# Performance work log

Measured on AMD Instinct MI355X. Metric: run time of the kernel, lower is better.

Reference implementation:

```python
import jax, jax.numpy as jnp
import numpy as np

R_MAX = 6.0
N_RADIAL = 5
N_BASIS = 7
N_SPECIES = 119
N_ATOMS = 25000
N_EDGES = 1000000


def _tril_2d(n):
    return np.array([(i, j) for i in range(n) for j in range(i + 1)], dtype=np.int32)


def _tril_3d(n):
    return np.array([(i, j, k) for i in range(n) for j in range(i + 1) for k in range(j + 1)], dtype=np.int32)


TRIL2 = jnp.asarray(_tril_2d(N_RADIAL))  # [15, 2]
TRIL3 = jnp.asarray(_tril_3d(N_RADIAL))  # [35, 3]


def setup_inputs() -> dict:
    key = jax.random.key(0)
    k1, k2, k3, k4 = jax.random.split(key, 4)
    dr_vec = jax.random.normal(k1, (N_EDGES, 3), jnp.float32) * 2.0
    Z = jax.random.randint(k2, (N_ATOMS,), 0, N_SPECIES, jnp.int32)
    neighbor_idxs = jax.random.randint(k3, (2, N_EDGES), 0, N_ATOMS, jnp.int32)
    coeffs = jax.random.normal(k4, (N_SPECIES, N_SPECIES, N_RADIAL, N_BASIS), jnp.float32) * 0.1
    return {"dr_vec": dr_vec, "Z": Z, "neighbor_idxs": neighbor_idxs, "coeffs": coeffs}


def _radial(dr, Z_i, Z_j, coeffs):
    # Gaussian basis (apax-style) with species-pair linear coefficients + cosine cutoff
    betta = N_BASIS ** 2 / R_MAX ** 2
    rad_norm = (2.0 * betta / np.pi) ** 0.75
    shifts = jnp.linspace(0.0, R_MAX, N_BASIS, dtype=dr.dtype)
    basis = rad_norm * jnp.exp(-betta * (dr[:, None] - shifts[None, :]) ** 2)  # [E, B]
    cutoff = 0.5 * (jnp.cos(np.pi * dr / R_MAX) + 1.0) * (dr < R_MAX)  # [E]
    c = coeffs[Z_i, Z_j]  # [E, R, B]
    rad = jnp.einsum("eb,erb->er", basis, c) * cutoff[:, None] / np.sqrt(N_BASIS)
    return rad  # [E, R]


def _forward(dr_vec, Z, neighbor_idxs, coeffs):
    idx_i, idx_j = neighbor_idxs[0], neighbor_idxs[1]
    Z_i, Z_j = Z[idx_i], Z[idx_j]
    dr = jnp.linalg.norm(dr_vec, axis=-1)  # [E]
    dn = dr_vec / (dr + 1e-5)[:, None]  # [E, 3]
    rad = _radial(dr, Z_i, Z_j, coeffs)  # [E, R]

    # per-edge outer-product moments
    m1e = rad[..., None] * dn[:, None, :]                      # [E,R,3]
    m2e = m1e[..., None] * dn[:, None, None, :]                # [E,R,3,3]
    m3e = m2e[..., None] * dn[:, None, None, None, :]          # [E,R,3,3,3]

    seg = lambda x: jax.ops.segment_sum(x, idx_j, num_segments=N_ATOMS)
    m0 = seg(rad)   # [A,R]
    m1 = seg(m1e)   # [A,R,3]
    m2 = seg(m2e)   # [A,R,3,3]
    m3 = seg(m3e)   # [A,R,3,3,3]

    contr_0 = m0
    contr_1 = jnp.einsum("ari,asi->rsa", m1, m1)
    contr_2 = jnp.einsum("arij,asij->rsa", m2, m2)
    contr_3 = jnp.einsum("arijk,asijk->rsa", m3, m3)
    contr_4 = jnp.einsum("arij,asik,atjk->rsta", m2, m2, m2)
    contr_5 = jnp.einsum("ari,asj,atij->rsta", m1, m1, m2)
    contr_6 = jnp.einsum("arijk,asijl,atkl->rsta", m3, m3, m2)
    contr_7 = jnp.einsum("arijk,asij,atk->rsta", m3, m2, m1)

    t2i, t2j = TRIL2[:, 0], TRIL2[:, 1]
    t3i, t3j, t3k = TRIL3[:, 0], TRIL3[:, 1], TRIL3[:, 2]

    n_atoms = contr_0.shape[0]
    contr_1 = contr_1[t2i, t2j].reshape(n_atoms, -1)
    contr_2 = contr_2[t2i, t2j].reshape(n_atoms, -1)
    contr_3 = contr_3[t2i, t2j].reshape(n_atoms, -1)
    contr_4 = contr_4[t3i, t3j, t3k].reshape(n_atoms, -1)
    contr_5 = contr_5[t2i, t2j].reshape(n_atoms, -1)
    contr_6 = contr_6[t2i, t2j].reshape(n_atoms, -1)
    contr_7 = contr_7.reshape(n_atoms, -1)

    return jnp.concatenate([contr_0, contr_1, contr_2, contr_3, contr_4, contr_5, contr_6, contr_7], axis=-1)


def reference(dr_vec, Z, neighbor_idxs, coeffs):
    return _forward(dr_vec, Z, neighbor_idxs, coeffs)
```

## Files before the change

### kernel.cpp

```cpp
#include <hip/hip_runtime.h>
#include <math.h>

#define NR 5
#define NB 7
#define NS 119
#define NA 25000
#define NE 1000000
#define OC 360
#define MUS 100
#define CAPR 96
#define CAPI 112
#define CHUNK 64
#define MPAD 101
#define CROW 36

static constexpr int T2I[15] = {0,1,1,2,2,2,3,3,3,3,4,4,4,4,4};
static constexpr int T2J[15] = {0,0,1,0,1,2,0,1,2,3,0,1,2,3,4};
static constexpr int T3I[35] = {0,1,1,1,2,2,2,2,2,2,3,3,3,3,3,3,3,3,3,3,4,4,4,4,4,4,4,4,4,4,4,4,4,4,4};
static constexpr int T3J[35] = {0,0,1,1,0,1,1,2,2,2,0,1,1,2,2,2,3,3,3,3,0,1,1,2,2,2,3,3,3,3,4,4,4,4,4};
static constexpr int T3K[35] = {0,0,0,1,0,0,1,0,1,2,0,0,1,0,1,2,0,1,2,3,0,0,1,0,1,2,0,1,2,3,0,1,2,3,4};

static constexpr int P2[9]  = {0,1,2, 1,3,4, 2,4,5};
static constexpr int P3[27] = {0,1,4, 1,2,5, 4,5,7,
                               1,2,5, 2,3,6, 5,6,8,
                               4,5,7, 5,6,8, 7,8,9};
static constexpr float W2[6]  = {1.f,2.f,2.f,1.f,2.f,1.f};
static constexpr float W3[10] = {1.f,3.f,3.f,1.f,3.f,6.f,3.f,3.f,3.f,1.f};

__global__ __launch_bounds__(256) void transpose_coeffs_kernel(
    const float* __restrict__ src, float* __restrict__ dst)
{
    int t = blockIdx.x * 256 + threadIdx.x;
    const int TOT = NS * NS * (NR * NB);
    if (t >= TOT) return;
    int pair = t / 35, rem = t - pair * 35;
    dst[pair * CROW + rem] = src[t];
}

__global__ __launch_bounds__(256) void edge_record_kernel(
    const float* __restrict__ dr_vec, const int* __restrict__ Z,
    const int* __restrict__ nbr, const float* __restrict__ coeffsT,
    int* __restrict__ cursor, float* __restrict__ binrec)
{
    int e = blockIdx.x * 256 + threadIdx.x;
    if (e >= NE) return;

    int aj = nbr[NE + e];
    int pos = __hip_atomic_fetch_add(&cursor[aj], 1,
                                     __ATOMIC_RELAXED, __HIP_MEMORY_SCOPE_AGENT);

    int ai = nbr[e];
    float x = dr_vec[3*e+0], y = dr_vec[3*e+1], z = dr_vec[3*e+2];
    int Zi = Z[ai], Zj = Z[aj];

    const float4* c4 = (const float4*)(coeffsT + (size_t)(Zi*NS + Zj) * CROW);
    float4 cw[9];
#pragma unroll
    for (int k = 0; k < 9; k++) cw[k] = c4[k];
    const float* cf = (const float*)&cw[0];

    float dr  = sqrtf(x*x + y*y + z*z);
    float inv = 1.0f / (dr + 1e-5f);
    float d0 = x*inv, d1 = y*inv, d2 = z*inv;

    const float PI_F = 3.14159265358979323846f;
    const float betta = 49.0f / 36.0f;
    float rad_norm = powf(2.0f * betta / PI_F, 0.75f);
    float cut = (dr < 6.0f) ? 0.5f*(cosf(PI_F * dr * (1.0f/6.0f)) + 1.0f) : 0.0f;
    float scale = cut * 0.3779644730092272272f;

    float basis[NB];
#pragma unroll
    for (int b = 0; b < NB; b++) {
        float t = dr - (float)b;
        basis[b] = rad_norm * expf(-betta * t * t);
    }

    float rad[NR];
#pragma unroll
    for (int r = 0; r < NR; r++) {
        float s = 0.f;
#pragma unroll
        for (int b = 0; b < NB; b++) s += basis[b] * cf[r*NB + b];
        rad[r] = s * scale;
    }

    if (pos < CAPR) {
        float4* rp = (float4*)(binrec + ((size_t)aj * CAPR + pos) * 8);
        rp[0] = make_float4(rad[0], rad[1], rad[2], rad[3]);
        rp[1] = make_float4(rad[4], d0, d1, d2);
    }
}

__global__ __launch_bounds__(256) void accum_contract_kernel(
    const int* __restrict__ cursor, const float* __restrict__ binrec,
    float* __restrict__ out)
{
    __shared__ float lds[CHUNK * MPAD];
    int base = blockIdx.x * CHUNK;
    int nat  = min(CHUNK, NA - base);

    int al  = threadIdx.x >> 2;
    int sub = threadIdx.x & 3;
    int a   = base + al;
    int n   = (a < NA) ? min(cursor[a], CAPR) : 0;

    float acc[MUS];
#pragma unroll
    for (int i = 0; i < MUS; i++) acc[i] = 0.f;

    const float* mybin = binrec + (size_t)a * CAPR * 8;
    for (int p = sub; p < n; p += 4) {
        const float4* rp = (const float4*)(mybin + (size_t)p * 8);
        float4 r0 = rp[0], r1 = rp[1];
        float rad[NR] = {r0.x, r0.y, r0.z, r0.w, r1.x};
        float d0 = r1.y, d1 = r1.z, d2 = r1.w;

        float q2[6] = {d0*d0, d1*d0, d2*d0, d1*d1, d2*d1, d2*d2};
        float q3[10] = {d0*q2[0], d1*q2[0], d0*q2[3], d1*q2[3], d2*q2[0],
                        d2*q2[1], d2*q2[3], d0*q2[5], d1*q2[5], d2*q2[5]};

#pragma unroll
        for (int r = 0; r < NR; r++) {
            float rv = rad[r];
            acc[r] += rv;
            acc[5 + r*3 + 0] += rv*d0;
            acc[5 + r*3 + 1] += rv*d1;
            acc[5 + r*3 + 2] += rv*d2;
#pragma unroll
            for (int q = 0; q < 6; q++)  acc[20 + r*6  + q] += rv*q2[q];
#pragma unroll
            for (int q = 0; q < 10; q++) acc[50 + r*10 + q] += rv*q3[q];
        }
    }

#pragma unroll
    for (int i = 0; i < MUS; i++) {
        float v = acc[i];
        v += __shfl_xor(v, 1, 64);
        v += __shfl_xor(v, 2, 64);
        if (sub == 0) lds[al * MPAD + i] = v;
    }
    __syncthreads();

    int wave = threadIdx.x >> 6, lane = threadIdx.x & 63;
    int a2 = base + lane;
    bool valid = (lane < nat);
    int mb = lane * MPAD;

#define ML(o) lds[mb + (o)]

    for (int cc = wave; cc < 360; cc += 4) {
        if (!valid) continue;
        float v; int dest;

        if (cc < 5) {
            v = ML(cc);
            dest = a2 * OC + cc;
        } else if (cc < 20) {
            int l = cc - 5;
            int r = T2I[l], s = T2J[l];
            float acc2 = 0.f;
#pragma unroll
            for (int i = 0; i < 3; i++) acc2 += ML(5 + r*3 + i) * ML(5 + s*3 + i);
            v = acc2;
            int f = l * NA + a2; int aa = f / 15; dest = aa * OC + 5 + (f - aa*15);
        } else if (cc < 35) {
            int l = cc - 20;
            int r = T2I[l], s = T2J[l];
            float acc2 = 0.f;
#pragma unroll
            for (int p = 0; p < 6; p++) acc2 += W2[p] * ML(20 + r*6 + p) * ML(20 + s*6 + p);
            v = acc2;
            int f = l * NA + a2; int aa = f / 15; dest = aa * OC + 20 + (f - aa*15);
        } else if (cc < 50) {
            int l = cc - 35;
            int r = T2I[l], s = T2J[l];
            float acc2 = 0.f;
#pragma unroll
            for (int p = 0; p < 10; p++) acc2 += W3[p] * ML(50 + r*10 + p) * ML(50 + s*10 + p);
            v = acc2;
            int f = l * NA + a2; int aa = f / 15; dest = aa * OC + 35 + (f - aa*15);
        } else if (cc < 85) {
            int l = cc - 50;
            int r = T3I[l], s = T3J[l], t = T3K[l];
            float R[6], S[6], T[6];
#pragma unroll
            for (int p = 0; p < 6; p++) { R[p]=ML(20+r*6+p); S[p]=ML(20+s*6+p); T[p]=ML(20+t*6+p); }
            float acc2 = 0.f;
#pragma unroll
            for (int i = 0; i < 3; i++)
#pragma unroll
            for (int j = 0; j < 3; j++)
#pragma unroll
            for (int k = 0; k < 3; k++)
                acc2 += R[P2[i*3+j]] * S[P2[i*3+k]] * T[P2[j*3+k]];
            v = acc2;
            int f = l * NA + a2; int aa = f / 35; dest = aa * OC + 50 + (f - aa*35);
        } else if (cc < 160) {
            int l = cc - 85;
            int p = l / 5, t = l - p*5;
            int r = T2I[p], s = T2J[p];
            float T[6];
#pragma unroll
            for (int q = 0; q < 6; q++) T[q] = ML(20 + t*6 + q);
            float acc2 = 0.f;
#pragma unroll
            for (int i = 0; i < 3; i++)
#pragma unroll
            for (int j = 0; j < 3; j++)
                acc2 += ML(5 + r*3 + i) * ML(5 + s*3 + j) * T[P2[i*3+j]];
            v = acc2;
            int f = l * NA + a2; int aa = f / 75; dest = aa * OC + 85 + (f - aa*75);
        } else if (cc < 235) {
            int l = cc - 160;
            int p = l / 5, t = l - p*5;
            int r = T2I[p], s = T2J[p];
            float R[10], S[10], T[6];
#pragma unroll
            for (int q = 0; q < 10; q++) { R[q]=ML(50+r*10+q); S[q]=ML(50+s*10+q); }
#pragma unroll
            for (int q = 0; q < 6;  q++) T[q] = ML(20 + t*6 + q);
            float acc2 = 0.f;
#pragma unroll
            for (int k = 0; k < 3; k++)
#pragma unroll
            for (int l2 = 0; l2 < 3; l2++) {
                float inner = 0.f;
#pragma unroll
                for (int i = 0; i < 3; i++)
#pragma unroll
                for (int j = 0; j < 3; j++)
                    inner += R[P3[(i*3+j)*3+k]] * S[P3[(i*3+j)*3+l2]];
                acc2 += inner * T[P2[k*3+l2]];
            }
            v = acc2;
            int f = l * NA + a2; int aa = f / 75; dest = aa * OC + 160 + (f - aa*75);
        } else {
            int l = cc - 235;
            int r = l / 25; int rem = l - r*25; int s = rem / 5; int t = rem - s*5;
            float R[10], S[6], T1[3];
#pragma unroll
            for (int q = 0; q < 10; q++) R[q] = ML(50 + r*10 + q);
#pragma unroll
            for (int q = 0; q < 6;  q++) S[q] = ML(20 + s*6 + q);
#pragma unroll
            for (int q = 0; q < 3;  q++) T1[q] = ML(5 + t*3 + q);
            float acc2 = 0.f;
#pragma unroll
            for (int i = 0; i < 3; i++)
#pragma unroll
            for (int j = 0; j < 3; j++)
#pragma unroll
            for (int k = 0; k < 3; k++)
                acc2 += R[P3[(i*3+j)*3+k]] * S[P2[i*3+j]] * T1[k];
            v = acc2;
            int f = l * NA + a2; int aa = f / 125; dest = aa * OC + 235 + (f - aa*125);
        }
        out[dest] = v;
    }
#undef ML
}

__global__ __launch_bounds__(256) void scatter_kernel(
    const int* __restrict__ nbr, int* __restrict__ cursor, int* __restrict__ bins)
{
    int e = blockIdx.x * 256 + threadIdx.x;
    if (e >= NE) return;
    int aj = nbr[NE + e];
    int pos = __hip_atomic_fetch_add(&cursor[aj], 1, __ATOMIC_RELAXED, __HIP_MEMORY_SCOPE_AGENT);
    if (pos < CAPI) bins[(size_t)aj * CAPI + pos] = e;
}

__global__ __launch_bounds__(256) void accum_kernel(
    const float* __restrict__ dr_vec, const int* __restrict__ Z,
    const int* __restrict__ nbr, const float* __restrict__ coeffs,
    const int* __restrict__ cursor, const int* __restrict__ bins,
    float* __restrict__ Mu)
{
    __shared__ float red[32 * MUS];
    int t   = blockIdx.x * 256 + threadIdx.x;
    int a   = t >> 3;
    int sub = t & 7;
    int al  = threadIdx.x >> 3;
    int n   = (a < NA) ? min(cursor[a], CAPI) : 0;
    int Zj  = (a < NA) ? Z[a] : 0;

    float acc[MUS];
#pragma unroll
    for (int i = 0; i < MUS; i++) acc[i] = 0.f;

    const int* mybin = bins + (size_t)a * CAPI;
    const float PI_F = 3.14159265358979323846f;
    const float betta = 49.0f / 36.0f;
    float rad_norm = powf(2.0f * betta / PI_F, 0.75f);

    for (int p = sub; p < n; p += 8) {
        int e = mybin[p];
        float x = dr_vec[3*e+0], y = dr_vec[3*e+1], z = dr_vec[3*e+2];
        int Zi = Z[nbr[e]];

        float dr  = sqrtf(x*x + y*y + z*z);
        float inv = 1.0f / (dr + 1e-5f);
        float d0 = x*inv, d1 = y*inv, d2 = z*inv;

        float cut = (dr < 6.0f) ? 0.5f*(cosf(PI_F * dr * (1.0f/6.0f)) + 1.0f) : 0.0f;
        float scale = cut * 0.3779644730092272272f;

        float basis[NB];
#pragma unroll
        for (int b = 0; b < NB; b++) {
            float tt = dr - (float)b;
            basis[b] = rad_norm * expf(-betta * tt * tt);
        }

        const float* cp = coeffs + ((size_t)(Zi*NS + Zj)) * (NR*NB);
        float rad[NR];
#pragma unroll
        for (int r = 0; r < NR; r++) {
            float s = 0.f;
#pragma unroll
            for (int b = 0; b < NB; b++) s += basis[b] * cp[r*NB + b];
            rad[r] = s * scale;
        }

        float q2[6] = {d0*d0, d1*d0, d2*d0, d1*d1, d2*d1, d2*d2};
        float q3[10] = {d0*q2[0], d1*q2[0], d0*q2[3], d1*q2[3], d2*q2[0],
                        d2*q2[1], d2*q2[3], d0*q2[5], d1*q2[5], d2*q2[5]};

#pragma unroll
        for (int r = 0; r < NR; r++) {
            float rv = rad[r];
            acc[r] += rv;
            acc[5 + r*3 + 0] += rv*d0;
            acc[5 + r*3 + 1] += rv*d1;
            acc[5 + r*3 + 2] += rv*d2;
#pragma unroll
            for (int q = 0; q < 6; q++)  acc[20 + r*6  + q] += rv*q2[q];
#pragma unroll
            for (int q = 0; q < 10; q++) acc[50 + r*10 + q] += rv*q3[q];
        }
    }

#pragma unroll
    for (int i = 0; i < MUS; i++) {
        float v = acc[i];
        v += __shfl_xor(v, 1, 64);
        v += __shfl_xor(v, 2, 64);
        v += __shfl_xor(v, 4, 64);
        if (sub == 0) red[al * MUS + i] = v;
    }
    __syncthreads();

    for (int u = threadIdx.x; u < 32 * MUS; u += 256) {
        int ga = blockIdx.x * 32 + u / MUS;
        if (ga < NA) Mu[(size_t)ga * MUS + (u - (u / MUS) * MUS)] = red[u];
    }
}

__global__ __launch_bounds__(256) void contract_kernel(
    const float* __restrict__ Mu, float* __restrict__ out)
{
    __shared__ float lds[CHUNK * MPAD];
    int base = blockIdx.x * CHUNK;
    int nat  = min(CHUNK, NA - base);

    for (int t = threadIdx.x; t < nat * MUS; t += 256) {
        int al = t / MUS, off = t - al * MUS;
        lds[al * MPAD + off] = Mu[(size_t)base * MUS + t];
    }
    __syncthreads();

    int wave = threadIdx.x >> 6, lane = threadIdx.x & 63;
    int a2 = base + lane;
    bool valid = (lane < nat);
    int mb = lane * MPAD;

#define ML(o) lds[mb + (o)]

    for (int cc = wave; cc < 360; cc += 4) {
        if (!valid) continue;
        float v; int dest;

        if (cc < 5) {
            v = ML(cc);
            dest = a2 * OC + cc;
        } else if (cc < 20) {
            int l = cc - 5;
            int r = T2I[l], s = T2J[l];
            float acc = 0.f;
#pragma unroll
            for (int i = 0; i < 3; i++) acc += ML(5 + r*3 + i) * ML(5 + s*3 + i);
            v = acc;
            int f = l * NA + a2; int aa = f / 15; dest = aa * OC + 5 + (f - aa*15);
        } else if (cc < 35) {
            int l = cc - 20;
            int r = T2I[l], s = T2J[l];
            float acc = 0.f;
#pragma unroll
            for (int p = 0; p < 6; p++) acc += W2[p] * ML(20 + r*6 + p) * ML(20 + s*6 + p);
            v = acc;
            int f = l * NA + a2; int aa = f / 15; dest = aa * OC + 20 + (f - aa*15);
        } else if (cc < 50) {
            int l = cc - 35;
            int r = T2I[l], s = T2J[l];
            float acc = 0.f;
#pragma unroll
            for (int p = 0; p < 10; p++) acc += W3[p] * ML(50 + r*10 + p) * ML(50 + s*10 + p);
            v = acc;
            int f = l * NA + a2; int aa = f / 15; dest = aa * OC + 35 + (f - aa*15);
        } else if (cc < 85) {
            int l = cc - 50;
            int r = T3I[l], s = T3J[l], t = T3K[l];
            float R[6], S[6], T[6];
#pragma unroll
            for (int p = 0; p < 6; p++) { R[p]=ML(20+r*6+p); S[p]=ML(20+s*6+p); T[p]=ML(20+t*6+p); }
            float acc = 0.f;
#pragma unroll
            for (int i = 0; i < 3; i++)
#pragma unroll
            for (int j = 0; j < 3; j++)
#pragma unroll
            for (int k = 0; k < 3; k++)
                acc += R[P2[i*3+j]] * S[P2[i*3+k]] * T[P2[j*3+k]];
            v = acc;
            int f = l * NA + a2; int aa = f / 35; dest = aa * OC + 50 + (f - aa*35);
        } else if (cc < 160) {
            int l = cc - 85;
            int p = l / 5, t = l - p*5;
            int r = T2I[p], s = T2J[p];
            float T[6];
#pragma unroll
            for (int q = 0; q < 6; q++) T[q] = ML(20 + t*6 + q);
            float acc = 0.f;
#pragma unroll
            for (int i = 0; i < 3; i++)
#pragma unroll
            for (int j = 0; j < 3; j++)
                acc += ML(5 + r*3 + i) * ML(5 + s*3 + j) * T[P2[i*3+j]];
            v = acc;
            int f = l * NA + a2; int aa = f / 75; dest = aa * OC + 85 + (f - aa*75);
        } else if (cc < 235) {
            int l = cc - 160;
            int p = l / 5, t = l - p*5;
            int r = T2I[p], s = T2J[p];
            float R[10], S[10], T[6];
#pragma unroll
            for (int q = 0; q < 10; q++) { R[q]=ML(50+r*10+q); S[q]=ML(50+s*10+q); }
#pragma unroll
            for (int q = 0; q < 6;  q++) T[q] = ML(20 + t*6 + q);
            float acc = 0.f;
#pragma unroll
            for (int k = 0; k < 3; k++)
#pragma unroll
            for (int l2 = 0; l2 < 3; l2++) {
                float inner = 0.f;
#pragma unroll
                for (int i = 0; i < 3; i++)
#pragma unroll
                for (int j = 0; j < 3; j++)
                    inner += R[P3[(i*3+j)*3+k]] * S[P3[(i*3+j)*3+l2]];
                acc += inner * T[P2[k*3+l2]];
            }
            v = acc;
            int f = l * NA + a2; int aa = f / 75; dest = aa * OC + 160 + (f - aa*75);
        } else {
            int l = cc - 235;
            int r = l / 25; int rem = l - r*25; int s = rem / 5; int t = rem - s*5;
            float R[10], S[6], T1[3];
#pragma unroll
            for (int q = 0; q < 10; q++) R[q] = ML(50 + r*10 + q);
#pragma unroll
            for (int q = 0; q < 6;  q++) S[q] = ML(20 + s*6 + q);
#pragma unroll
            for (int q = 0; q < 3;  q++) T1[q] = ML(5 + t*3 + q);
            float acc = 0.f;
#pragma unroll
            for (int i = 0; i < 3; i++)
#pragma unroll
            for (int j = 0; j < 3; j++)
#pragma unroll
            for (int k = 0; k < 3; k++)
                acc += R[P3[(i*3+j)*3+k]] * S[P2[i*3+j]] * T1[k];
            v = acc;
            int f = l * NA + a2; int aa = f / 125; dest = aa * OC + 235 + (f - aa*125);
        }
        out[dest] = v;
    }
#undef ML
}

extern "C" void kernel_launch(void* const* d_in, const int* in_sizes, int n_in,
                              void* d_out, int out_size, void* d_ws, size_t ws_size,
                              hipStream_t stream) {
    const float* dr_vec = (const float*)d_in[0];
    const int*   Z      = (const int*)d_in[1];
    const int*   nbr    = (const int*)d_in[2];
    const float* coeffs = (const float*)d_in[3];
    float* out = (float*)d_out;

    size_t need_fast = (size_t)NA * sizeof(int)
                     + (size_t)NS * NS * CROW * sizeof(float)
                     + (size_t)NA * CAPR * 8 * sizeof(float);

    if (ws_size >= need_fast) {
        int*   cursor  = (int*)d_ws;
        float* coeffsT = (float*)(cursor + NA);
        float* binrec  = coeffsT + (size_t)NS * NS * CROW;
        hipMemsetAsync(cursor, 0, (size_t)NA * sizeof(int), stream);
        const int TOT = NS * NS * (NR * NB);
        transpose_coeffs_kernel<<<(TOT + 255)/256, 256, 0, stream>>>(coeffs, coeffsT);
        edge_record_kernel<<<(NE + 255)/256, 256, 0, stream>>>(dr_vec, Z, nbr, coeffsT, cursor, binrec);
        accum_contract_kernel<<<(NA + CHUNK - 1)/CHUNK, 256, 0, stream>>>(cursor, binrec, out);
    } else {
        int*   cursor = (int*)d_ws;
        int*   bins   = cursor + NA;
        float* Mu     = (float*)(bins + (size_t)NA * CAPI);
        hipMemsetAsync(cursor, 0, (size_t)NA * sizeof(int), stream);
        scatter_kernel<<<(NE + 255)/256, 256, 0, stream>>>(nbr, cursor, bins);
        accum_kernel<<<(NA*8 + 255)/256, 256, 0, stream>>>(dr_vec, Z, nbr, coeffs, cursor, bins, Mu);
        contract_kernel<<<(NA + CHUNK - 1)/CHUNK, 256, 0, stream>>>(Mu, out);
    }
}
```

Measured before the change: 209.2 us.

## Replace fixed-capacity atomic bins with counting-sort CSR layout for edge records

Swaps the per-atom global atomic cursor and fixed 96-slot bins for a counting sort. A per-block LDS histogram with 16-bit packed counters feeds a column scan and a base scan, and a scatter kernel then writes each edge record into a compact CSR slot. This removes global atomics and the padded, sparsely filled bin array, so the accumulate pass reads contiguous records, and it drops the silent cap on edges per atom. The cost is three extra kernel launches, a single-block serial scan, and a 256x12500 partial table (about 12.8 MB each for hist and partial) that must be written and read.

Result: slower. 251.1 us (+20.0%).

```diff
diff --git a/kernel.cpp b/kernel.cpp
--- a/kernel.cpp
+++ b/kernel.cpp
@@ -8,11 +8,14 @@
 #define NE 1000000
 #define OC 360
 #define MUS 100
-#define CAPR 96
 #define CAPI 112
 #define CHUNK 64
 #define MPAD 101
 #define CROW 36
+
+#define NB_BLK 256
+#define CH 3907
+#define NPAIR 12500
 
 static constexpr int T2I[15] = {0,1,1,2,2,2,3,3,3,3,4,4,4,4,4};
 static constexpr int T2J[15] = {0,0,1,0,1,2,0,1,2,3,0,1,2,3,4};
@@ -27,6 +30,7 @@
 static constexpr float W2[6]  = {1.f,2.f,2.f,1.f,2.f,1.f};
 static constexpr float W3[10] = {1.f,3.f,3.f,1.f,3.f,6.f,3.f,3.f,3.f,1.f};
 
+
 __global__ __launch_bounds__(256) void transpose_coeffs_kernel(
     const float* __restrict__ src, float* __restrict__ dst)
 {
@@ -37,79 +41,147 @@
     dst[pair * CROW + rem] = src[t];
 }
 
-__global__ __launch_bounds__(256) void edge_record_kernel(
+__global__ __launch_bounds__(1024) void hist_kernel(
+    const int* __restrict__ nbr, unsigned int* __restrict__ hist)
+{
+    __shared__ unsigned int h[NPAIR];
+    int b = blockIdx.x;
+    for (int i = threadIdx.x; i < NPAIR; i += 1024) h[i] = 0u;
+    __syncthreads();
+    int e0 = b * CH, e1 = min(NE, e0 + CH);
+    for (int e = e0 + (int)threadIdx.x; e < e1; e += 1024) {
+        int aj = nbr[NE + e];
+        atomicAdd(&h[aj >> 1], 1u << ((aj & 1) * 16));
+    }
+    __syncthreads();
+    unsigned int* out = hist + (size_t)b * NPAIR;
+    for (int i = threadIdx.x; i < NPAIR; i += 1024) out[i] = h[i];
+}
+
+__global__ __launch_bounds__(256) void colscan_kernel(
+    const unsigned int* __restrict__ hist, unsigned int* __restrict__ partial,
+    unsigned int* __restrict__ colsum)
+{
+    int t = blockIdx.x * 256 + threadIdx.x;
+    if (t >= NPAIR) return;
+    unsigned int run = 0u;
+    for (int b = 0; b < NB_BLK; b++) {
+        unsigned int v = hist[(size_t)b * NPAIR + t];
+        partial[(size_t)b * NPAIR + t] = run;
+        run += v;
+    }
+    colsum[t] = run;
+}
+
+__global__ __launch_bounds__(256) void basescan_kernel(
+    const unsigned int* __restrict__ colsum, unsigned int* __restrict__ base)
+{
+    __shared__ unsigned int tot[256];
+    int t = threadIdx.x;
+    const int PPT = (NPAIR + 255) / 256;
+    int p0 = t * PPT, p1 = min(NPAIR, p0 + PPT);
+    unsigned int s = 0u;
+    for (int p = p0; p < p1; p++) {
+        unsigned int v = colsum[p];
+        s += (v & 0xFFFFu) + (v >> 16);
+    }
+    tot[t] = s;
+    __syncthreads();
+    for (int off = 1; off < 256; off <<= 1) {
+        unsigned int v = (t >= off) ? tot[t - off] : 0u;
+        __syncthreads();
+        if (t >= off) tot[t] += v;
+        __syncthreads();
+    }
+    unsigned int run = tot[t] - s;
+    for (int p = p0; p < p1; p++) {
+        unsigned int v = colsum[p];
+        base[2*p]     = run; run += (v & 0xFFFFu);
+        base[2*p + 1] = run; run += (v >> 16);
+    }
+    if (t == 255) base[NA] = run;
+}
+
+__global__ __launch_bounds__(1024) void sortscatter_kernel(
     const float* __restrict__ dr_vec, const int* __restrict__ Z,
     const int* __restrict__ nbr, const float* __restrict__ coeffsT,
-    int* __restrict__ cursor, float* __restrict__ binrec)
-{
-    int e = blockIdx.x * 256 + threadIdx.x;
-    if (e >= NE) return;
-
-    int aj = nbr[NE + e];
-    int pos = __hip_atomic_fetch_add(&cursor[aj], 1,
-                                     __ATOMIC_RELAXED, __HIP_MEMORY_SCOPE_AGENT);
-
-    int ai = nbr[e];
-    float x = dr_vec[3*e+0], y = dr_vec[3*e+1], z = dr_vec[3*e+2];
-    int Zi = Z[ai], Zj = Z[aj];
-
-    const float4* c4 = (const float4*)(coeffsT + (size_t)(Zi*NS + Zj) * CROW);
-    float4 cw[9];
-#pragma unroll
-    for (int k = 0; k < 9; k++) cw[k] = c4[k];
-    const float* cf = (const float*)&cw[0];
-
-    float dr  = sqrtf(x*x + y*y + z*z);
-    float inv = 1.0f / (dr + 1e-5f);
-    float d0 = x*inv, d1 = y*inv, d2 = z*inv;
-
-    const float PI_F = 3.14159265358979323846f;
-    const float betta = 49.0f / 36.0f;
-    float rad_norm = powf(2.0f * betta / PI_F, 0.75f);
-    float cut = (dr < 6.0f) ? 0.5f*(cosf(PI_F * dr * (1.0f/6.0f)) + 1.0f) : 0.0f;
-    float scale = cut * 0.3779644730092272272f;
-
-    float basis[NB];
-#pragma unroll
-    for (int b = 0; b < NB; b++) {
-        float t = dr - (float)b;
-        basis[b] = rad_norm * expf(-betta * t * t);
-    }
-
-    float rad[NR];
-#pragma unroll
-    for (int r = 0; r < NR; r++) {
-        float s = 0.f;
-#pragma unroll
-        for (int b = 0; b < NB; b++) s += basis[b] * cf[r*NB + b];
-        rad[r] = s * scale;
-    }
-
-    if (pos < CAPR) {
-        float4* rp = (float4*)(binrec + ((size_t)aj * CAPR + pos) * 8);
+    const unsigned int* __restrict__ partial, const unsigned int* __restrict__ base,
+    float* __restrict__ binrec)
+{
+    __shared__ unsigned int ctr[NPAIR];
+    int b = blockIdx.x;
+    const unsigned int* prow = partial + (size_t)b * NPAIR;
+    for (int i = threadIdx.x; i < NPAIR; i += 1024) ctr[i] = prow[i];
+    __syncthreads();
+
+    int e0 = b * CH, e1 = min(NE, e0 + CH);
+    for (int e = e0 + (int)threadIdx.x; e < e1; e += 1024) {
+        int aj = nbr[NE + e];
+        int sh = (aj & 1) * 16;
+        unsigned int old = atomicAdd(&ctr[aj >> 1], 1u << sh);
+        unsigned int slot = base[aj] + ((old >> sh) & 0xFFFFu);
+
+        int ai = nbr[e];
+        float x = dr_vec[3*e+0], y = dr_vec[3*e+1], z = dr_vec[3*e+2];
+        int Zi = Z[ai], Zj = Z[aj];
+
+        const float4* c4 = (const float4*)(coeffsT + (size_t)(Zi*NS + Zj) * CROW);
+        float4 cw[9];
+#pragma unroll
+        for (int k = 0; k < 9; k++) cw[k] = c4[k];
+        const float* cf = (const float*)&cw[0];
+
+        float dr  = sqrtf(x*x + y*y + z*z);
+        float inv = 1.0f / (dr + 1e-5f);
+        float d0 = x*inv, d1 = y*inv, d2 = z*inv;
+
+        const float PI_F = 3.14159265358979323846f;
+        const float betta = 49.0f / 36.0f;
+        float rad_norm = powf(2.0f * betta / PI_F, 0.75f);
+        float cut = (dr < 6.0f) ? 0.5f*(cosf(PI_F * dr * (1.0f/6.0f)) + 1.0f) : 0.0f;
+        float scale = cut * 0.3779644730092272272f;
+
+        float basis[NB];
+#pragma unroll
+        for (int q = 0; q < NB; q++) {
+            float tt = dr - (float)q;
+            basis[q] = rad_norm * expf(-betta * tt * tt);
+        }
+
+        float rad[NR];
+#pragma unroll
+        for (int r = 0; r < NR; r++) {
+            float s = 0.f;
+#pragma unroll
+            for (int q = 0; q < NB; q++) s += basis[q] * cf[r*NB + q];
+            rad[r] = s * scale;
+        }
+
+        float4* rp = (float4*)(binrec + (size_t)slot * 8);
         rp[0] = make_float4(rad[0], rad[1], rad[2], rad[3]);
         rp[1] = make_float4(rad[4], d0, d1, d2);
     }
 }
 
 __global__ __launch_bounds__(256) void accum_contract_kernel(
-    const int* __restrict__ cursor, const float* __restrict__ binrec,
+    const unsigned int* __restrict__ base, const float* __restrict__ binrec,
     float* __restrict__ out)
 {
     __shared__ float lds[CHUNK * MPAD];
-    int base = blockIdx.x * CHUNK;
-    int nat  = min(CHUNK, NA - base);
+    int bl = blockIdx.x * CHUNK;
+    int nat  = min(CHUNK, NA - bl);
 
     int al  = threadIdx.x >> 2;
     int sub = threadIdx.x & 3;
-    int a   = base + al;
-    int n   = (a < NA) ? min(cursor[a], CAPR) : 0;
+    int a   = bl + al;
+    unsigned int b0 = 0u; int n = 0;
+    if (a < NA) { b0 = base[a]; n = (int)(base[a+1] - b0); }
 
     float acc[MUS];
 #pragma unroll
     for (int i = 0; i < MUS; i++) acc[i] = 0.f;
 
-    const float* mybin = binrec + (size_t)a * CAPR * 8;
+    const float* mybin = binrec + (size_t)b0 * 8;
     for (int p = sub; p < n; p += 4) {
         const float4* rp = (const float4*)(mybin + (size_t)p * 8);
         float4 r0 = rp[0], r1 = rp[1];
@@ -144,7 +216,7 @@
     __syncthreads();
 
     int wave = threadIdx.x >> 6, lane = threadIdx.x & 63;
-    int a2 = base + lane;
+    int a2 = bl + lane;
     bool valid = (lane < nat);
     int mb = lane * MPAD;
 
@@ -361,9 +433,9 @@
 __global__ __launch_bounds__(256) void contract_kernel(
     const float* __restrict__ Mu, float* __restrict__ out)
 {
-    __shared__ float lds[CHUNK * MPAD];
-    int base = blockIdx.x * CHUNK;
-    int nat  = min(CHUNK, NA - base);
+    __shared__ float lds[64 * MPAD];
+    int base = blockIdx.x * 64;
+    int nat  = min(64, NA - base);
 
     for (int t = threadIdx.x; t < nat * MUS; t += 256) {
         int al = t / MUS, off = t - al * MUS;
@@ -499,19 +571,31 @@
     const float* coeffs = (const float*)d_in[3];
     float* out = (float*)d_out;
 
-    size_t need_fast = (size_t)NA * sizeof(int)
-                     + (size_t)NS * NS * CROW * sizeof(float)
-                     + (size_t)NA * CAPR * 8 * sizeof(float);
+    auto aup = [](size_t x) { return (x + 255) & ~(size_t)255; };
+    size_t off_binrec  = 0;
+    size_t off_hist    = aup(off_binrec + (size_t)NE * 8 * sizeof(float));
+    size_t off_partial = aup(off_hist + (size_t)NB_BLK * NPAIR * sizeof(unsigned int));
+    size_t off_colsum  = aup(off_partial + (size_t)NB_BLK * NPAIR * sizeof(unsigned int));
+    size_t off_base    = aup(off_colsum + (size_t)NPAIR * sizeof(unsigned int));
+    size_t off_coefT   = aup(off_base + (size_t)(NA + 1) * sizeof(unsigned int));
+    size_t need_fast   = off_coefT + (size_t)NS * NS * CROW * sizeof(float);
 
     if (ws_size >= need_fast) {
-        int*   cursor  = (int*)d_ws;
-        float* coeffsT = (float*)(cursor + NA);
-        float* binrec  = coeffsT + (size_t)NS * NS * CROW;
-        hipMemsetAsync(cursor, 0, (size_t)NA * sizeof(int), stream);
+        char* w = (char*)d_ws;
+        float*        binrec  = (float*)(w + off_binrec);
+        unsigned int* hist    = (unsigned int*)(w + off_hist);
+        unsigned int* partial = (unsigned int*)(w + off_partial);
+        unsigned int* colsum  = (unsigned int*)(w + off_colsum);
+        unsigned int* base    = (unsigned int*)(w + off_base);
+        float*        coeffsT = (float*)(w + off_coefT);
+
         const int TOT = NS * NS * (NR * NB);
         transpose_coeffs_kernel<<<(TOT + 255)/256, 256, 0, stream>>>(coeffs, coeffsT);
-        edge_record_kernel<<<(NE + 255)/256, 256, 0, stream>>>(dr_vec, Z, nbr, coeffsT, cursor, binrec);
-        accum_contract_kernel<<<(NA + CHUNK - 1)/CHUNK, 256, 0, stream>>>(cursor, binrec, out);
+        hist_kernel<<<NB_BLK, 1024, 0, stream>>>(nbr, hist);
+        colscan_kernel<<<(NPAIR + 255)/256, 256, 0, stream>>>(hist, partial, colsum);
+        basescan_kernel<<<1, 256, 0, stream>>>(colsum, base);
+        sortscatter_kernel<<<NB_BLK, 1024, 0, stream>>>(dr_vec, Z, nbr, coeffsT, partial, base, binrec);
+        accum_contract_kernel<<<(NA + CHUNK - 1)/CHUNK, 256, 0, stream>>>(base, binrec, out);
     } else {
         int*   cursor = (int*)d_ws;
         int*   bins   = cursor + NA;
@@ -519,6 +603,6 @@
         hipMemsetAsync(cursor, 0, (size_t)NA * sizeof(int), stream);
         scatter_kernel<<<(NE + 255)/256, 256, 0, stream>>>(nbr, cursor, bins);
         accum_kernel<<<(NA*8 + 255)/256, 256, 0, stream>>>(dr_vec, Z, nbr, coeffs, cursor, bins, Mu);
-        contract_kernel<<<(NA + CHUNK - 1)/CHUNK, 256, 0, stream>>>(Mu, out);
-    }
-}
+        contract_kernel<<<(NA + 63)/64, 256, 0, stream>>>(Mu, out);
+    }
+}
```
